# Performance work log

Measured on AMD Instinct MI355X. Metric: run time of the kernel, lower is better.

Reference implementation:

```python
import jax, jax.numpy as jnp
import numpy as np

EMBED = 1024
HEADS = 16
HEAD_DIM = EMBED // HEADS
B, S = 2, 2048


def setup_inputs() -> dict:
    key = jax.random.key(0)
    ks = jax.random.split(key, 13)
    def lin(kw, kb):
        # torch nn.Linear default init: U(-1/sqrt(fan_in), 1/sqrt(fan_in))
        bound = 1.0 / np.sqrt(EMBED)
        W = jax.random.uniform(kw, (EMBED, EMBED), jnp.float32, -bound, bound)
        b = jax.random.uniform(kb, (EMBED,), jnp.float32, -bound, bound)
        return W, b
    Wq, bq = lin(ks[0], ks[1])
    Wk, bk = lin(ks[2], ks[3])
    Wv, bv = lin(ks[4], ks[5])
    Wo, bo = lin(ks[6], ks[7])
    return {
        "query": jax.random.normal(ks[8], (B, S, EMBED), jnp.float32),
        "key": jax.random.normal(ks[9], (B, S, EMBED), jnp.float32),
        "value": jax.random.normal(ks[10], (B, S, EMBED), jnp.float32),
        "mask": jax.random.randint(ks[11], (B, S, S), 0, 2, jnp.int32),
        "Wq": Wq, "bq": bq, "Wk": Wk, "bk": bk,
        "Wv": Wv, "bv": bv, "Wo": Wo, "bo": bo,
    }


def _split_heads(x):
    b, s, _ = x.shape
    return x.reshape(b, s, HEADS, HEAD_DIM).transpose(0, 2, 1, 3)  # [B,H,S,D]


def reference(query, key, value, mask, Wq, bq, Wk, bk, Wv, bv, Wo, bo):
    scaling = HEAD_DIM ** -0.5
    q = _split_heads(query @ Wq.T + bq) * scaling          # [B,H,Sq,D]
    k = _split_heads(key @ Wk.T + bk)                       # [B,H,Sk,D]
    v = _split_heads(value @ Wv.T + bv)                     # [B,H,Sk,D]
    scores = jnp.einsum('bhqd,bhkd->bhqk', q, k)            # [B,H,Sq,Sk]
    scores = jnp.where(mask[:, None, :, :] == 0, jnp.float32(-10000.0), scores)
    p = jax.nn.softmax(scores, axis=-1)
    x = jnp.einsum('bhqk,bhkd->bhqd', p, v)                 # [B,H,Sq,D]
    b, h, s, d = x.shape
    x = x.transpose(0, 2, 1, 3).reshape(b, s, h * d)
    return x @ Wo.T + bo
```

## Files before the change

### kernel.cpp

```cpp
#include <hip/hip_runtime.h>

#define EMBED 1024
#define HEADS 16
#define HDIM  64
#define BATCH 2
#define SEQ   2048
#define MTOT  (BATCH*SEQ)
#define LOG2E 1.4426950408889634f
#define QSCALE (0.125f * LOG2E)

typedef __attribute__((ext_vector_type(8)))  short short8;
typedef __attribute__((ext_vector_type(4)))  float f32x4;
typedef __attribute__((ext_vector_type(16))) float f32x16;

#define MFMA(a,b,c)   __builtin_amdgcn_mfma_f32_16x16x32_bf16(a,b,c,0,0,0)
#define MFMA32(a,b,c) __builtin_amdgcn_mfma_f32_32x32x16_bf16(a,b,c,0,0,0)

__device__ __forceinline__ ushort f2bf(float f) {
  union { float f; unsigned u; } v; v.f = f;
  unsigned u = v.u;
  unsigned r = u + 0x7fffu + ((u >> 16) & 1u);
  return (ushort)(r >> 16);
}
__device__ __forceinline__ unsigned packbf(float a, float b) {
  return (unsigned)f2bf(a) | ((unsigned)f2bf(b) << 16);
}
__device__ __forceinline__ unsigned cvtpk(float lo, float hi) {
  unsigned r;
  asm("v_cvt_pk_bf16_f32 %0, %1, %2" : "=v"(r) : "v"(lo), "v"(hi));
  return r;
}
__device__ __forceinline__ uint2 cvt4(float4 v) {
  uint2 r;
  asm("v_cvt_pk_bf16_f32 %0, %2, %3\n\t"
      "v_cvt_pk_bf16_f32 %1, %4, %5"
      : "=&v"(r.x), "=&v"(r.y)
      : "v"(v.x), "v"(v.y), "v"(v.z), "v"(v.w));
  return r;
}
__device__ __forceinline__ void gl_lds16(const ushort* g, ushort* l) {
  __builtin_amdgcn_global_load_lds(
      (const __attribute__((address_space(1))) unsigned*)g,
      (__attribute__((address_space(3))) unsigned*)l, 16, 0, 0);
}

__global__ __launch_bounds__(256) void tobf16(
    const float* __restrict__ s0, const float* __restrict__ s1, const float* __restrict__ s2,
    const float* __restrict__ s3, const float* __restrict__ s4, const float* __restrict__ s5,
    const float* __restrict__ s6,
    ushort* __restrict__ d0, ushort* __restrict__ d1, ushort* __restrict__ d2,
    ushort* __restrict__ d3, ushort* __restrict__ d4, ushort* __restrict__ d5,
    ushort* __restrict__ d6)
{
  const int z = blockIdx.z;
  const float* s; ushort* d;
  switch (z) {
    case 0: s = s0; d = d0; break;
    case 1: s = s1; d = d1; break;
    case 2: s = s2; d = d2; break;
    case 3: s = s3; d = d3; break;
    case 4: s = s4; d = d4; break;
    case 5: s = s5; d = d5; break;
    default: s = s6; d = d6; break;
  }
  const int nch = (z < 3) ? (MTOT * EMBED / 8) : (EMBED * EMBED / 8);
  int i = blockIdx.x * 256 + threadIdx.x;
  if (i >= nch) return;
  float4 a = reinterpret_cast<const float4*>(s)[2 * i];
  float4 b = reinterpret_cast<const float4*>(s)[2 * i + 1];
  uint2 lo = cvt4(a), hi = cvt4(b);
  reinterpret_cast<uint4*>(d)[i] = make_uint4(lo.x, lo.y, hi.x, hi.y);
}

__global__ __launch_bounds__(256) void maskpack(const int* __restrict__ mask,
                                                unsigned long long* __restrict__ bits) {
  size_t idx = (size_t)blockIdx.x * 256 + threadIdx.x;
  unsigned long long bal = __ballot(mask[idx] != 0);
  if ((threadIdx.x & 63) == 0) bits[idx >> 6] = bal;
}

template<int OM>
__global__ __launch_bounds__(512, 4) void gemm_bf(
    const ushort* __restrict__ A0, const ushort* __restrict__ A1, const ushort* __restrict__ A2,
    const ushort* __restrict__ W0, const ushort* __restrict__ W1, const ushort* __restrict__ W2,
    const float* __restrict__ b0, const float* __restrict__ b1, const float* __restrict__ b2,
    ushort* __restrict__ oq, ushort* __restrict__ ok, ushort* __restrict__ ov,
    float* __restrict__ of)
{
  __shared__ __align__(16) ushort lds[2][2][8192];

  const int nwg = (OM == 0) ? 768 : 256;
  int lin = blockIdx.x + (blockIdx.y << 3);
  int swz = (lin & 7) * (nwg >> 3) + (lin >> 3);
  const int z  = swz >> 8;
  const int r_ = swz & 255;
  const int n0 = (r_ & 7) << 7;
  const int m0 = (r_ >> 3) << 7;

  const ushort* __restrict__ A    = (z == 0) ? A0 : (z == 1) ? A1 : A2;
  const ushort* __restrict__ W    = (z == 0) ? W0 : (z == 1) ? W1 : W2;
  const float*  __restrict__ bias = (z == 0) ? b0 : (z == 1) ? b1 : b2;

  const int t = threadIdx.x;
  const int lane = t & 63;
  const int wid = t >> 6;
  const int wr = wid >> 2, wc = wid & 3;
  const int lr = lane & 15, qg = lane >> 4;

  auto stage = [&](int buf, int k0) {
    #pragma unroll
    for (int it = 0; it < 2; ++it) {
      int idx = it * 512 + t;
      int row = idx >> 3;
      int col = ((idx & 7) ^ (row & 7)) << 3;
      gl_lds16(&A[(size_t)(m0 + row) * EMBED + k0 + col], &lds[buf][0][idx * 8]);
    }
    #pragma unroll
    for (int it = 0; it < 2; ++it) {
      int idx = it * 512 + t;
      int row = idx >> 3;
      int col = ((idx & 7) ^ (row & 7)) << 3;
      gl_lds16(&W[(size_t)(n0 + row) * EMBED + k0 + col], &lds[buf][1][idx * 8]);
    }
  };

  f32x4 acc[4][2] = {};

  stage(0, 0);
  asm volatile("s_waitcnt vmcnt(0)" ::: "memory");
  __syncthreads();

  for (int kt = 0; kt < 16; ++kt) {
    const int buf = kt & 1;
    if (kt < 15) stage(buf ^ 1, (kt + 1) * 64);

    #pragma unroll
    for (int ks = 0; ks < 2; ++ks) {
      short8 af[4], bfr[2];
      #pragma unroll
      for (int mi = 0; mi < 4; ++mi) {
        int row = wr * 64 + mi * 16 + lr;
        int cp = (ks * 4 + qg) ^ (row & 7);
        af[mi] = *reinterpret_cast<const short8*>(&lds[buf][0][row * 64 + (cp << 3)]);
      }
      #pragma unroll
      for (int ni = 0; ni < 2; ++ni) {
        int row = wc * 32 + ni * 16 + lr;
        int cp = (ks * 4 + qg) ^ (row & 7);
        bfr[ni] = *reinterpret_cast<const short8*>(&lds[buf][1][row * 64 + (cp << 3)]);
      }
      __builtin_amdgcn_s_setprio(1);
      #pragma unroll
      for (int mi = 0; mi < 4; ++mi)
        #pragma unroll
        for (int ni = 0; ni < 2; ++ni)
          acc[mi][ni] = MFMA(af[mi], bfr[ni], acc[mi][ni]);
      __builtin_amdgcn_s_setprio(0);
    }

    if (kt < 15) {
      asm volatile("s_waitcnt vmcnt(0)" ::: "memory");
      __syncthreads();
    }
  }

  #pragma unroll
  for (int ni = 0; ni < 2; ++ni) {
    int ng = n0 + wc * 32 + ni * 16 + lr;
    float bv_ = bias[ng];
    int h = ng >> 6, d = ng & 63;
    #pragma unroll
    for (int mi = 0; mi < 4; ++mi) {
      #pragma unroll
      for (int r = 0; r < 4; ++r) {
        int mg = m0 + wr * 64 + mi * 16 + qg * 4 + r;
        float val = acc[mi][ni][r] + bv_;
        if (OM == 1) {
          of[(size_t)mg * EMBED + ng] = val;
        } else {
          int bb = mg >> 11, s = mg & (SEQ - 1);
          int bh = bb * HEADS + h;
          if (z == 0)
            oq[((size_t)bh * SEQ + s) * HDIM + d] = f2bf(val * QSCALE);
          else if (z == 1)
            ok[((size_t)bh * SEQ + s) * HDIM + d] = f2bf(val);
          else {
            size_t addr = (((size_t)bh * 2 + (d >> 5)) * (SEQ / 32) + (s >> 5)) * 1024
                        + (size_t)(d & 31) * 32 + (s & 31);
            ov[addr] = f2bf(val);
          }
        }
      }
    }
  }
}

__global__ __launch_bounds__(256, 2) void attn(
    const ushort* __restrict__ qws, const ushort* __restrict__ kws,
    const ushort* __restrict__ vws, const unsigned* __restrict__ mbits,
    ushort* __restrict__ xws)
{
  const int t = threadIdx.x;
  const int wid = t >> 6;
  const int l = t & 63;
  const int q31 = l & 31;
  const int h = l >> 5;

  const int L = blockIdx.x;
  const int j = L >> 3;
  const int bh = ((L & 7) << 2) + (j >> 4);
  const int q0 = (j & 15) << 7;
  const int b = bh >> 4, head = bh & 15;

  __shared__ __align__(16) ushort lds[9216];

  const int qrow = q0 + wid * 32 + q31;
  const ushort* qp = qws + ((size_t)bh * SEQ + qrow) * HDIM + 8 * h;
  short8 qf[4];
  #pragma unroll
  for (int s = 0; s < 4; ++s)
    qf[s] = *reinterpret_cast<const short8*>(qp + 16 * s);

  const int rp = (q31 & 19) | ((q31 & 4) << 1) | ((q31 & 8) >> 1);

  int koff[4];
  #pragma unroll
  for (int i = 0; i < 4; ++i)
    koff[i] = rp * 64 + (((h + 2 * i) ^ (rp & 7)) << 3);
  int voff[2][2];
  #pragma unroll
  for (int sb = 0; sb < 2; ++sb)
    #pragma unroll
    for (int jj = 0; jj < 2; ++jj)
      voff[sb][jj] = sb * 1024 + q31 * 32 + (((h + 2 * jj) ^ ((q31 >> 1) & 3)) << 3);

  const ushort* ksb = kws + (size_t)bh * SEQ * HDIM
                    + ((t >> 3) << 6) + (((t & 7) ^ ((t >> 3) & 7)) << 3);
  const int vsub = t >> 7, vd = (t >> 2) & 31, vc = t & 3;
  const ushort* vsb = vws + (((size_t)bh * 2 + vsub) << 16)
                    + vd * 32 + ((vc ^ ((vd >> 1) & 3)) << 3);
  ushort* kd0 = lds + t * 8;
  ushort* vd0 = lds + 2048 + t * 8;

  const unsigned* mp = mbits + (size_t)(b * SEQ + qrow) * (SEQ / 32);

  f32x16 accT[2] = {};
  float ls0 = 0.f, ls1 = 0.f, ls2 = 0.f, ls3 = 0.f;

  auto STAGE = [&](int tile, int bb) {
    gl_lds16(ksb + (size_t)tile * 2048, kd0 + bb);
    gl_lds16(vsb + (size_t)tile * 1024, vd0 + bb);
  };

  auto COMP = [&](int bb, unsigned mwc) {
    const ushort* kb = lds + bb;
    const ushort* vb = lds + bb + 2048;
    short8 kf0 = *reinterpret_cast<const short8*>(kb + koff[0]);
    short8 kf1 = *reinterpret_cast<const short8*>(kb + koff[1]);
    short8 kf2 = *reinterpret_cast<const short8*>(kb + koff[2]);
    short8 kf3 = *reinterpret_cast<const short8*>(kb + koff[3]);
    __builtin_amdgcn_s_setprio(1);
    f32x16 s = {};
    s = MFMA32(kf0, qf[0], s);
    s = MFMA32(kf1, qf[1], s);
    s = MFMA32(kf2, qf[2], s);
    s = MFMA32(kf3, qf[3], s);
    __builtin_amdgcn_s_setprio(0);

    short8 vf0 = *reinterpret_cast<const short8*>(vb + voff[0][0]);
    short8 vf1 = *reinterpret_cast<const short8*>(vb + voff[0][1]);
    short8 vf2 = *reinterpret_cast<const short8*>(vb + voff[1][0]);
    short8 vf3 = *reinterpret_cast<const short8*>(vb + voff[1][1]);

    unsigned msh = mwc >> (8 * h);
    union U { unsigned u[4]; short8 s8; } p0u, p1u;
    #pragma unroll
    for (int i = 0; i < 8; ++i) {
      const int r0 = 2 * i, r1 = 2 * i + 1;
      float e0 = ((msh >> ((r0 & 7) + 16 * (r0 >> 3))) & 1u) ? __builtin_amdgcn_exp2f(s[r0]) : 0.0f;
      float e1 = ((msh >> ((r1 & 7) + 16 * (r1 >> 3))) & 1u) ? __builtin_amdgcn_exp2f(s[r1]) : 0.0f;
      if ((i & 3) == 0) ls0 += e0 + e1;
      else if ((i & 3) == 1) ls1 += e0 + e1;
      else if ((i & 3) == 2) ls2 += e0 + e1;
      else ls3 += e0 + e1;
      if (i < 4) p0u.u[i] = cvtpk(e0, e1);
      else       p1u.u[i - 4] = cvtpk(e0, e1);
    }

    __builtin_amdgcn_s_setprio(1);
    accT[0] = MFMA32(vf0, p0u.s8, accT[0]);
    accT[0] = MFMA32(vf1, p1u.s8, accT[0]);
    accT[1] = MFMA32(vf2, p0u.s8, accT[1]);
    accT[1] = MFMA32(vf3, p1u.s8, accT[1]);
    __builtin_amdgcn_s_setprio(0);
  };

  unsigned mw = *mp; ++mp;
  STAGE(0, 0);
  asm volatile("s_waitcnt vmcnt(0)" ::: "memory");
  __syncthreads();

  #pragma unroll 1
  for (int it = 0; it < 32; ++it) {
    STAGE(2 * it + 1, 4096);
    unsigned mn = *mp; ++mp;
    COMP(0, mw);
    asm volatile("s_waitcnt vmcnt(0)" ::: "memory");
    __syncthreads();
    mw = mn;
    if (it < 31) STAGE(2 * it + 2, 0);
    mn = *mp; ++mp;
    COMP(4096, mw);
    asm volatile("s_waitcnt vmcnt(0)" ::: "memory");
    __syncthreads();
    mw = mn;
  }

  float lsum = (ls0 + ls1) + (ls2 + ls3);
  float lrow = lsum + __shfl_xor(lsum, 32);
  float inv = 1.0f / lrow;

  ushort* xb = lds + wid * 2304;
  #pragma unroll
  for (int nb = 0; nb < 2; ++nb)
    #pragma unroll
    for (int rg = 0; rg < 4; ++rg) {
      int dbase = 32 * nb + 8 * rg + 4 * h;
      uint2 pk = make_uint2(
          packbf(accT[nb][4 * rg] * inv,     accT[nb][4 * rg + 1] * inv),
          packbf(accT[nb][4 * rg + 2] * inv, accT[nb][4 * rg + 3] * inv));
      *reinterpret_cast<uint2*>(&xb[q31 * 72 + dbase]) = pk;
    }
  asm volatile("" ::: "memory");
  #pragma unroll
  for (int pp = 0; pp < 4; ++pp) {
    int row = pp * 8 + (l >> 3);
    int col = (l & 7) * 8;
    short8 xv = *reinterpret_cast<const short8*>(&xb[row * 72 + col]);
    *reinterpret_cast<short8*>(
        &xws[((size_t)b * SEQ + q0 + wid * 32 + row) * EMBED + head * HDIM + col]) = xv;
  }
}

extern "C" void kernel_launch(void* const* d_in, const int* in_sizes, int n_in,
                              void* d_out, int out_size, void* d_ws, size_t ws_size,
                              hipStream_t stream) {
  (void)in_sizes; (void)n_in; (void)out_size; (void)ws_size;
  const float* query = (const float*)d_in[0];
  const float* key   = (const float*)d_in[1];
  const float* value = (const float*)d_in[2];
  const int*   mask  = (const int*)d_in[3];
  const float* Wq = (const float*)d_in[4];  const float* bq = (const float*)d_in[5];
  const float* Wk = (const float*)d_in[6];  const float* bk = (const float*)d_in[7];
  const float* Wv = (const float*)d_in[8];  const float* bv = (const float*)d_in[9];
  const float* Wo = (const float*)d_in[10]; const float* bo = (const float*)d_in[11];
  float* out = (float*)d_out;

  const size_t NQKV = (size_t)BATCH * HEADS * SEQ * HDIM;
  const size_t NW   = (size_t)EMBED * EMBED;
  ushort* qws = (ushort*)d_ws;
  ushort* kws = qws + NQKV;
  ushort* vws = kws + NQKV;
  ushort* xws = vws + NQKV;
  unsigned* mbits = (unsigned*)(xws + NQKV);
  ushort* aqb = (ushort*)(mbits + (size_t)BATCH * SEQ * SEQ / 32);
  ushort* akb = aqb + NQKV;
  ushort* avb = akb + NQKV;
  ushort* wqb = avb + NQKV;
  ushort* wkb = wqb + NW;
  ushort* wvb = wkb + NW;
  ushort* wob = wvb + NW;

  tobf16<<<dim3((NQKV / 8 + 255) / 256, 1, 7), 256, 0, stream>>>(
      query, key, value, Wq, Wk, Wv, Wo, aqb, akb, avb, wqb, wkb, wvb, wob);

  maskpack<<<(BATCH * SEQ * SEQ) / 256, 256, 0, stream>>>(mask, (unsigned long long*)mbits);

  gemm_bf<0><<<dim3(8, 96), 512, 0, stream>>>(
      aqb, akb, avb, wqb, wkb, wvb, bq, bk, bv, qws, kws, vws, nullptr);

  attn<<<dim3(512), 256, 0, stream>>>(qws, kws, vws, mbits, xws);

  gemm_bf<1><<<dim3(8, 32), 512, 0, stream>>>(
      xws, xws, xws, wob, wob, wob, bo, bo, bo, qws, kws, vws, out);
}
```

Measured before the change: 148.9 us.

## Use 256x256-tile QKV projection GEMM with 4-stage LDS pipeline

Replaces the templated 128-wide QKV projection GEMM with a dedicated kernel that computes 256x256 output tiles per workgroup. It uses a 4-buffer prefetch pipeline three stages deep. Larger tiles raise arithmetic intensity and cut redundant global loads of A and W. The cost is 192 workgroups on a 256-CU device, which underfills the machine, plus higher register and LDS pressure (occupancy 2).

```diff
diff --git a/kernel.cpp b/kernel.cpp
--- a/kernel.cpp
+++ b/kernel.cpp
@@ -77,6 +77,119 @@
   size_t idx = (size_t)blockIdx.x * 256 + threadIdx.x;
   unsigned long long bal = __ballot(mask[idx] != 0);
   if ((threadIdx.x & 63) == 0) bits[idx >> 6] = bal;
+}
+
+__global__ __launch_bounds__(512, 2) void gemm_qkv256(
+    const ushort* __restrict__ A0, const ushort* __restrict__ A1, const ushort* __restrict__ A2,
+    const ushort* __restrict__ W0, const ushort* __restrict__ W1, const ushort* __restrict__ W2,
+    const float* __restrict__ b0, const float* __restrict__ b1, const float* __restrict__ b2,
+    ushort* __restrict__ oq, ushort* __restrict__ ok, ushort* __restrict__ ov)
+{
+  __shared__ __align__(16) ushort lds[4][2][8192];
+
+  const int nwg = 192;
+  int lin = blockIdx.x;
+  int swz = (lin & 7) * (nwg >> 3) + (lin >> 3);
+  const int z  = swz >> 6;
+  const int r_ = swz & 63;
+  const int n0 = (r_ & 3) << 8;
+  const int m0 = (r_ >> 2) << 8;
+
+  const ushort* __restrict__ A    = (z == 0) ? A0 : (z == 1) ? A1 : A2;
+  const ushort* __restrict__ W    = (z == 0) ? W0 : (z == 1) ? W1 : W2;
+  const float*  __restrict__ bias = (z == 0) ? b0 : (z == 1) ? b1 : b2;
+
+  const int t = threadIdx.x;
+  const int lane = t & 63;
+  const int wid = t >> 6;
+  const int wr = wid >> 2, wc = wid & 3;
+  const int lr = lane & 15, qg = lane >> 4;
+
+  auto stage = [&](int buf, int k0) {
+    #pragma unroll
+    for (int it = 0; it < 2; ++it) {
+      int idx = it * 512 + t;
+      int row = idx >> 2;
+      int col = (((idx & 3) - (row >> 1)) & 3) << 3;
+      gl_lds16(&A[(size_t)(m0 + row) * EMBED + k0 + col], &lds[buf][0][idx * 8]);
+    }
+    #pragma unroll
+    for (int it = 0; it < 2; ++it) {
+      int idx = it * 512 + t;
+      int row = idx >> 2;
+      int col = (((idx & 3) - (row >> 1)) & 3) << 3;
+      gl_lds16(&W[(size_t)(n0 + row) * EMBED + k0 + col], &lds[buf][1][idx * 8]);
+    }
+  };
+
+  f32x4 acc[8][4] = {};
+
+  stage(0, 0);
+  stage(1, 32);
+  stage(2, 64);
+  asm volatile("s_waitcnt vmcnt(8)" ::: "memory");
+  __builtin_amdgcn_s_barrier();
+  asm volatile("" ::: "memory");
+
+  for (int kt = 0; kt < 32; ++kt) {
+    const int buf = kt & 3;
+    if (kt < 29) stage((kt + 3) & 3, (kt + 3) * 32);
+
+    const ushort* ab = &lds[buf][0][0];
+    const ushort* bb = &lds[buf][1][0];
+    short8 bfr[4];
+    #pragma unroll
+    for (int ni = 0; ni < 4; ++ni) {
+      int row = wc * 64 + ni * 16 + lr;
+      int sidx = (qg + (row >> 1)) & 3;
+      bfr[ni] = *reinterpret_cast<const short8*>(bb + row * 32 + (sidx << 3));
+    }
+    #pragma unroll
+    for (int mi = 0; mi < 8; ++mi) {
+      int row = wr * 128 + mi * 16 + lr;
+      int sidx = (qg + (row >> 1)) & 3;
+      short8 af = *reinterpret_cast<const short8*>(ab + row * 32 + (sidx << 3));
+      __builtin_amdgcn_s_setprio(1);
+      #pragma unroll
+      for (int ni = 0; ni < 4; ++ni)
+        acc[mi][ni] = MFMA(af, bfr[ni], acc[mi][ni]);
+      __builtin_amdgcn_s_setprio(0);
+    }
+
+    if (kt < 31) {
+      if (kt < 29)       asm volatile("s_waitcnt vmcnt(8)" ::: "memory");
+      else if (kt == 29) asm volatile("s_waitcnt vmcnt(4)" ::: "memory");
+      else               asm volatile("s_waitcnt vmcnt(0)" ::: "memory");
+      __builtin_amdgcn_s_barrier();
+      asm volatile("" ::: "memory");
+    }
+  }
+
+  #pragma unroll
+  for (int ni = 0; ni < 4; ++ni) {
+    int ng = n0 + wc * 64 + ni * 16 + lr;
+    float bv_ = bias[ng];
+    int h = ng >> 6, d = ng & 63;
+    #pragma unroll
+    for (int mi = 0; mi < 8; ++mi) {
+      #pragma unroll
+      for (int r = 0; r < 4; ++r) {
+        int mg = m0 + wr * 128 + mi * 16 + qg * 4 + r;
+        float val = acc[mi][ni][r] + bv_;
+        int bb_ = mg >> 11, s = mg & (SEQ - 1);
+        int bh = bb_ * HEADS + h;
+        if (z == 0)
+          oq[((size_t)bh * SEQ + s) * HDIM + d] = f2bf(val * QSCALE);
+        else if (z == 1)
+          ok[((size_t)bh * SEQ + s) * HDIM + d] = f2bf(val);
+        else {
+          size_t addr = (((size_t)bh * 2 + (d >> 5)) * (SEQ / 32) + (s >> 5)) * 1024
+                      + (size_t)(d & 31) * 32 + (s & 31);
+          ov[addr] = f2bf(val);
+        }
+      }
+    }
+  }
 }
 
 template<int OM>
@@ -376,8 +489,8 @@
 
   maskpack<<<(BATCH * SEQ * SEQ) / 256, 256, 0, stream>>>(mask, (unsigned long long*)mbits);
 
-  gemm_bf<0><<<dim3(8, 96), 512, 0, stream>>>(
-      aqb, akb, avb, wqb, wkb, wvb, bq, bk, bv, qws, kws, vws, nullptr);
+  gemm_qkv256<<<dim3(192), 512, 0, stream>>>(
+      aqb, akb, avb, wqb, wkb, wvb, bq, bk, bv, qws, kws, vws);
 
   attn<<<dim3(512), 256, 0, stream>>>(qws, kws, vws, mbits, xws);
 
```

Result: slower. 151.9 us (+2.0%).
